# Kernel tuning notes

Measured on AMD Instinct MI355X. Metric: run time of the kernel, lower is better.

The kernel has to match this reference:

```python
import jax, jax.numpy as jnp
import numpy as np

NUM_EXPERTS = 8
CAPACITY_FACTOR = 1.0
MIN_CAPACITY = 4


def setup_inputs() -> dict:
    key = jax.random.key(0)
    k0, k1, k2, k3 = jax.random.split(key, 4)
    B, S, M, F, E = 4, 2048, 2048, 8192, NUM_EXPERTS
    return {
        "hidden_states": jax.random.normal(k0, (B, S, M), jnp.float32),
        "wg": jax.random.normal(k1, (M, E), jnp.float32) * 0.02,
        "w1": jax.random.normal(k2, (E, M, F), jnp.float32) * 0.02,
        "b1": jnp.zeros((E, F), jnp.float32),
        "w2": jax.random.normal(k3, (E, F, M), jnp.float32) * 0.02,
        "b2": jnp.zeros((E, M), jnp.float32),
    }


def reference(hidden_states, wg, w1, b1, w2, b2):
    B, S, M = hidden_states.shape
    E = NUM_EXPERTS
    T = B * S  # total tokens
    x = hidden_states.reshape(T, M)

    # ---- top-1 gating (DeepSpeed top1gating, no noise / no RTS) ----
    logits = x @ wg                                  # [T, E]
    gates = jax.nn.softmax(logits, axis=-1)          # [T, E]
    capacity = max(int(np.ceil(T / E * CAPACITY_FACTOR)), MIN_CAPACITY)

    idx1 = jnp.argmax(gates, axis=1)                 # [T]
    mask1 = jax.nn.one_hot(idx1, E, dtype=gates.dtype)  # [T, E]

    # position of each token within its expert's queue
    locations1 = jnp.cumsum(mask1, axis=0) - 1.0     # [T, E]

    # load-balancing aux loss (computed before capacity drop)
    me = jnp.mean(gates, axis=0)
    ce = jnp.mean(mask1, axis=0)
    l_aux = jnp.sum(me * ce) * E

    # drop tokens beyond capacity
    mask1 = mask1 * (locations1 < capacity).astype(mask1.dtype)
    locations1_s = jnp.sum(locations1 * mask1, axis=1).astype(jnp.int32)  # [T]

    gates1 = gates * mask1                           # [T, E], zero for dropped tokens
    loc_sc = jax.nn.one_hot(locations1_s, capacity, dtype=gates.dtype)    # [T, C]

    combine_weights = jnp.einsum("se,sc->sec", gates1, loc_sc)            # [T, E, C]
    dispatch_mask = (combine_weights > 0).astype(x.dtype)                  # [T, E, C]

    # ---- dispatch -> grouped-GEMM experts -> combine ----
    dispatched = jnp.einsum("sec,sm->ecm", dispatch_mask, x)              # [E, C, M]
    h = jax.nn.gelu(jnp.einsum("ecm,emf->ecf", dispatched, w1) + b1[:, None, :])
    expert_out = jnp.einsum("ecf,efm->ecm", h, w2) + b2[:, None, :]       # [E, C, M]

    out = jnp.einsum("sec,ecm->sm", combine_weights, expert_out)          # [T, M]
    return out.reshape(B, S, M), l_aux
```

## Files before the change

### kernel.cpp

```cpp
#include <hip/hip_runtime.h>
#include <hip/hip_bf16.h>
#include <math.h>

#define T_TOK 8192
#define M_DIM 2048
#define F_DIM 8192
#define E_NUM 8
#define CAP   1024

typedef unsigned short u16;
typedef __attribute__((ext_vector_type(8))) short short8;
typedef __attribute__((ext_vector_type(4))) float f32x4;

__device__ __forceinline__ u16 f2bf(float f){
  unsigned int x = __builtin_bit_cast(unsigned int, f);
  unsigned int lsb = (x >> 16) & 1u;
  x += 0x7fffu + lsb;
  return (u16)(x >> 16);
}
__device__ __forceinline__ unsigned int pack2(float a, float b){
  return (unsigned int)f2bf(a) | ((unsigned int)f2bf(b) << 16);
}

typedef __attribute__((address_space(3))) unsigned int lds_uint;
typedef __attribute__((address_space(1))) const unsigned int g_uint;
__device__ __forceinline__ void gl_lds16(const u16* g, u16* l){
  __builtin_amdgcn_global_load_lds((g_uint*)g, (lds_uint*)l, 16, 0, 0);
}
typedef __attribute__((address_space(3))) u16 lds_u16;
__device__ __forceinline__ unsigned int lds_off(u16* p){
  return (unsigned int)(unsigned long long)(lds_u16*)p;
}

__device__ __forceinline__ float gelu_tanh(float v){
  float u = 0.7978845608028654f * (v + 0.044715f * v * v * v);
  return 0.5f * v * (1.0f + tanhf(u));
}

__device__ __forceinline__ size_t tiled_off(int e, int n, int k, int nt128, int nkt){
  return ((((size_t)e * nt128 + (n >> 7)) * nkt + (k >> 6)) * 2 + ((k >> 5) & 1)) * 4096
         + (size_t)((n & 127) * 32 + ((((k >> 3) & 3) ^ ((n >> 1) & 3)) << 3) + (k & 7));
}

__global__ __launch_bounds__(256) void gating_kernel(
    const float* __restrict__ x, const float* __restrict__ wg,
    int* __restrict__ expert_id, float* __restrict__ gate_val,
    float* __restrict__ mepart)
{
  int wave = threadIdx.x >> 6, lane = threadIdx.x & 63;
  int t = blockIdx.x * 4 + wave;
  float acc[8];
  #pragma unroll
  for (int e = 0; e < 8; ++e) acc[e] = 0.f;
  const float* xr = x + (size_t)t * M_DIM;
  for (int i = lane; i < M_DIM; i += 64) {
    float xv = xr[i];
    const float4* wr = (const float4*)(wg + (size_t)i * 8);
    float4 w0 = wr[0], w1v = wr[1];
    acc[0] += xv * w0.x;  acc[1] += xv * w0.y;  acc[2] += xv * w0.z;  acc[3] += xv * w0.w;
    acc[4] += xv * w1v.x; acc[5] += xv * w1v.y; acc[6] += xv * w1v.z; acc[7] += xv * w1v.w;
  }
  #pragma unroll
  for (int off = 32; off; off >>= 1)
    #pragma unroll
    for (int e = 0; e < 8; ++e) acc[e] += __shfl_xor(acc[e], off);

  float mx = acc[0]; int bi = 0;
  #pragma unroll
  for (int e = 1; e < 8; ++e) if (acc[e] > mx) { mx = acc[e]; bi = e; }
  float p[8]; float s = 0.f;
  #pragma unroll
  for (int e = 0; e < 8; ++e) { p[e] = expf(acc[e] - mx); s += p[e]; }
  float inv = 1.f / s;

  __shared__ float pl[4][8];
  if (lane == 0) {
    expert_id[t] = bi;
    gate_val[t] = p[bi] * inv;
    #pragma unroll
    for (int e = 0; e < 8; ++e) pl[wave][e] = p[e] * inv;
  }
  __syncthreads();
  if (threadIdx.x < 8) {
    float m = pl[0][threadIdx.x] + pl[1][threadIdx.x] + pl[2][threadIdx.x] + pl[3][threadIdx.x];
    mepart[blockIdx.x * 8 + threadIdx.x] = m;
  }
}

__global__ __launch_bounds__(1024) void scan_kernel(
    const int* __restrict__ expert_id, const float* __restrict__ gate_val,
    const float* __restrict__ mepart, int nmep,
    int* __restrict__ slot_token, float* __restrict__ slot_gate,
    float* __restrict__ laux_out)
{
  __shared__ int wcnt[16][8];
  __shared__ int base[8];
  __shared__ float red[128][8];
  int tid = threadIdx.x, wave = tid >> 6, lane = tid & 63;
  if (tid < 8) base[tid] = 0;

  int e0 = tid & 7, g = tid >> 3;
  float mesum = 0.f;
  for (int r = g; r < nmep; r += 128) mesum += mepart[r * 8 + e0];
  red[g][e0] = mesum;
  __syncthreads();

  for (int tile = 0; tile < T_TOK / 1024; ++tile) {
    int t = tile * 1024 + tid;
    int e = expert_id[t];
    int lp = 0;
    #pragma unroll
    for (int ee = 0; ee < 8; ++ee) {
      unsigned long long m = __ballot(e == ee);
      if (lane == 0) wcnt[wave][ee] = __popcll(m);
      if (ee == e)   lp = __popcll(m & ((1ull << lane) - 1ull));
    }
    __syncthreads();
    int wp = 0;
    for (int w2 = 0; w2 < wave; ++w2) wp += wcnt[w2][e];
    int pos = base[e] + wp + lp;
    if (pos < CAP) {
      slot_token[e * CAP + pos] = t;
      slot_gate[e * CAP + pos] = gate_val[t];
    }
    __syncthreads();
    if (tid < 8) {
      int s = 0;
      for (int w2 = 0; w2 < 16; ++w2) s += wcnt[w2][tid];
      base[tid] += s;
    }
    __syncthreads();
  }

  if (tid < 8) {
    float me = 0.f;
    for (int r = 0; r < 128; ++r) me += red[r][tid];
    me /= (float)T_TOK;
    float ce = (float)base[tid] / (float)T_TOK;
    red[0][tid] = me * ce;
  }
  __syncthreads();
  if (tid == 0) {
    float s = 0.f;
    for (int e = 0; e < 8; ++e) s += red[0][e];
    *laux_out = s * (float)E_NUM;
  }
}

__global__ __launch_bounds__(256) void transpose_cvt_kernel(
    const float* __restrict__ in, u16* __restrict__ out, int R, int Cc)
{
  __shared__ float tile[64][65];
  int e = blockIdx.z;
  const float* ine = in + (size_t)e * R * Cc;
  int r0 = blockIdx.y * 64, c0 = blockIdx.x * 64;
  int tr = threadIdx.x >> 4, tc = threadIdx.x & 15;
  #pragma unroll
  for (int it = 0; it < 4; ++it) {
    float4 v = *(const float4*)&ine[(size_t)(r0 + it * 16 + tr) * Cc + c0 + tc * 4];
    tile[it * 16 + tr][tc * 4 + 0] = v.x;
    tile[it * 16 + tr][tc * 4 + 1] = v.y;
    tile[it * 16 + tr][tc * 4 + 2] = v.z;
    tile[it * 16 + tr][tc * 4 + 3] = v.w;
  }
  __syncthreads();
  int nt128 = Cc >> 7, nkt = R >> 6;
  int oc = threadIdx.x >> 2, q = threadIdx.x & 3;
  int n = c0 + oc, k0 = r0 + q * 16;
  u16 vals[16];
  #pragma unroll
  for (int i = 0; i < 16; ++i) vals[i] = f2bf(tile[q * 16 + i][oc]);
  unsigned int w[8];
  #pragma unroll
  for (int i = 0; i < 8; ++i) w[i] = (unsigned int)vals[2 * i] | ((unsigned int)vals[2 * i + 1] << 16);
  uint4 pa; pa.x = w[0]; pa.y = w[1]; pa.z = w[2]; pa.w = w[3];
  uint4 pb; pb.x = w[4]; pb.y = w[5]; pb.z = w[6]; pb.w = w[7];
  *(uint4*)&out[tiled_off(e, n, k0,     nt128, nkt)] = pa;
  *(uint4*)&out[tiled_off(e, n, k0 + 8, nt128, nkt)] = pb;
}

__global__ __launch_bounds__(256) void dispatch_kernel(
    const float* __restrict__ x, const int* __restrict__ slot_token,
    u16* __restrict__ Xe)
{
  int slot = blockIdx.x;
  int e = slot >> 10, c = slot & (CAP - 1);
  int t = slot_token[slot];
  int m = threadIdx.x * 8;
  uint4 pk;
  if (t < 0) {
    pk.x = pk.y = pk.z = pk.w = 0u;
  } else {
    const float* xr = x + (size_t)t * M_DIM + m;
    float4 a = *(const float4*)xr;
    float4 b = *(const float4*)(xr + 4);
    pk.x = pack2(a.x, a.y); pk.y = pack2(a.z, a.w);
    pk.z = pack2(b.x, b.y); pk.w = pack2(b.z, b.w);
  }
  *(uint4*)&Xe[tiled_off(e, c, m, CAP >> 7, M_DIM >> 6)] = pk;
}

template<int MH, int GATE>
__device__ __forceinline__ void do_phase(
    unsigned aAddr, unsigned bAddr,
    short8 (&bfr)[4], f32x4 (&acc)[4][4],
    const u16* __restrict__ tb, u16* sreg, int skt, int skh,
    int tid, int wave)
{
  short8 af[2];
  unsigned aA = aAddr + MH * 2048;
  if (MH == 0) {
    asm volatile("ds_read_b128 %0, %1 offset:0"    : "=v"(bfr[0]) : "v"(bAddr));
    asm volatile("ds_read_b128 %0, %1 offset:1024" : "=v"(bfr[1]) : "v"(bAddr));
    asm volatile("ds_read_b128 %0, %1 offset:2048" : "=v"(bfr[2]) : "v"(bAddr));
    asm volatile("ds_read_b128 %0, %1 offset:3072" : "=v"(bfr[3]) : "v"(bAddr));
  }
  asm volatile("ds_read_b128 %0, %1 offset:0"    : "=v"(af[0]) : "v"(aA));
  asm volatile("ds_read_b128 %0, %1 offset:1024" : "=v"(af[1]) : "v"(aA));
  const u16* src = tb + ((size_t)(skt * 2 + skh) << 12);
  #pragma unroll
  for (int j = 0; j < 2; ++j)
    gl_lds16(src + (size_t)(j * 256 + tid) * 8, sreg + (j * 256 + (wave << 6)) * 8);
  __builtin_amdgcn_s_barrier();
  asm volatile("s_waitcnt lgkmcnt(0)");
  __builtin_amdgcn_sched_barrier(0);
  __builtin_amdgcn_s_setprio(1);
  #pragma unroll
  for (int m2 = 0; m2 < 2; ++m2)
    #pragma unroll
    for (int n2 = 0; n2 < 4; ++n2)
      acc[MH * 2 + m2][n2] = __builtin_amdgcn_mfma_f32_16x16x32_bf16(
          af[m2], bfr[n2], acc[MH * 2 + m2][n2], 0, 0, 0);
  __builtin_amdgcn_s_setprio(0);
  if (GATE) {
    asm volatile("s_waitcnt vmcnt(6)");
    __builtin_amdgcn_sched_barrier(0);
  }
  __builtin_amdgcn_s_barrier();
}

template<int EPI>
__global__ __launch_bounds__(256, 2) void gemm8_kernel(
    const u16* __restrict__ A,
    const u16* __restrict__ B,
    const float* __restrict__ bias,
    u16* __restrict__ Hout,
    float* __restrict__ Out,
    const int* __restrict__ slot_token, const float* __restrict__ slot_gate,
    int K, int NR)
{
  __shared__ __align__(16) u16 SA[2][2][4096];
  __shared__ __align__(16) u16 SB[2][2][4096];

  int e = blockIdx.z;
  int n0 = blockIdx.x * 128, m0 = blockIdx.y * 128;
  int nkt = K >> 6;
  const u16* Atb = A + (((size_t)(e * (CAP >> 7) + (m0 >> 7)) * nkt) * 2) * 4096;
  const u16* Btb = B + (((size_t)(e * (NR >> 7) + (n0 >> 7)) * nkt) * 2) * 4096;

  int tid = threadIdx.x, wave = tid >> 6, lane = tid & 63;
  int wr = wave >> 1, wc = wave & 1;
  int l15 = lane & 15, g2 = lane >> 4;

  int rs = (l15 >> 1) & 3;
  int cg = (g2 ^ rs) * 8;
  int arow_base = (wr * 64 + l15) * 32 + cg;
  int brow_base = (wc * 64 + l15) * 32 + cg;

  unsigned aAddr[2][2], bAddr[2][2];
  #pragma unroll
  for (int b = 0; b < 2; ++b)
    #pragma unroll
    for (int h = 0; h < 2; ++h) {
      aAddr[b][h] = lds_off(&SA[b][h][0]) + (unsigned)(arow_base * 2);
      bAddr[b][h] = lds_off(&SB[b][h][0]) + (unsigned)(brow_base * 2);
    }

  f32x4 acc[4][4];
  #pragma unroll
  for (int m = 0; m < 4; ++m)
    #pragma unroll
    for (int n = 0; n < 4; ++n)
      acc[m][n] = (f32x4){0.f, 0.f, 0.f, 0.f};
  short8 bfr[4];

  auto stage0 = [&](const u16* tb, u16* region, int kt, int kh) {
    const u16* src = tb + ((size_t)(kt * 2 + kh) << 12);
    #pragma unroll
    for (int j = 0; j < 2; ++j)
      gl_lds16(src + (size_t)(j * 256 + tid) * 8, region + (j * 256 + (wave << 6)) * 8);
  };

  int nk = K >> 6, ni = nk >> 1;
  stage0(Btb, &SB[0][0][0], 0, 0);
  stage0(Atb, &SA[0][0][0], 0, 0);
  stage0(Btb, &SB[0][1][0], 0, 1);
  stage0(Atb, &SA[0][1][0], 0, 1);
  stage0(Btb, &SB[1][0][0], 1, 0);
  stage0(Atb, &SA[1][0][0], 1, 0);
  stage0(Btb, &SB[1][1][0], 1, 1);
  asm volatile("s_waitcnt vmcnt(6)");
  __builtin_amdgcn_sched_barrier(0);
  __builtin_amdgcn_s_barrier();

  #pragma unroll 1
  for (int i = 0; i < ni; ++i) {
    int t1 = 2 * i + 1;
    int t2 = 2 * i + 2 < nk ? 2 * i + 2 : nk - 1;
    int t3 = 2 * i + 3 < nk ? 2 * i + 3 : nk - 1;
    do_phase<0,0>(aAddr[0][0], bAddr[0][0], bfr, acc, Atb, &SA[1][1][0], t1, 1, tid, wave);
    do_phase<1,0>(aAddr[0][0], bAddr[0][0], bfr, acc, Btb, &SB[0][0][0], t2, 0, tid, wave);
    do_phase<0,0>(aAddr[0][1], bAddr[0][1], bfr, acc, Atb, &SA[0][0][0], t2, 0, tid, wave);
    do_phase<1,1>(aAddr[0][1], bAddr[0][1], bfr, acc, Btb, &SB[0][1][0], t2, 1, tid, wave);
    do_phase<0,0>(aAddr[1][0], bAddr[1][0], bfr, acc, Atb, &SA[0][1][0], t2, 1, tid, wave);
    do_phase<1,0>(aAddr[1][0], bAddr[1][0], bfr, acc, Btb, &SB[1][0][0], t3, 0, tid, wave);
    do_phase<0,0>(aAddr[1][1], bAddr[1][1], bfr, acc, Atb, &SA[1][0][0], t3, 0, tid, wave);
    do_phase<1,1>(aAddr[1][1], bAddr[1][1], bfr, acc, Btb, &SB[1][1][0], t3, 1, tid, wave);
  }

  int wrb = wr * 64, wcb = wc * 64;
  const float* be = bias + (size_t)e * NR + n0;
  if (EPI == 0) {
    #pragma unroll
    for (int wm = 0; wm < 4; ++wm) {
      #pragma unroll
      for (int j = 0; j < 4; ++j) {
        int r = wrb + wm * 16 + g2 * 4 + j;
        #pragma unroll
        for (int n = 0; n < 4; ++n) {
          int c = wcb + n * 16 + l15;
          float v = acc[wm][n][j] + be[c];
          Hout[tiled_off(e, m0 + r, n0 + c, CAP >> 7, F_DIM >> 6)] = f2bf(gelu_tanh(v));
        }
      }
    }
  } else {
    #pragma unroll
    for (int wm = 0; wm < 4; ++wm) {
      #pragma unroll
      for (int j = 0; j < 4; ++j) {
        int r = wrb + wm * 16 + g2 * 4 + j;
        int slot = e * CAP + m0 + r;
        int tk = slot_token[slot];
        if (tk >= 0) {
          float gv = slot_gate[slot];
          size_t rowoff = (size_t)tk * M_DIM + n0;
          #pragma unroll
          for (int n = 0; n < 4; ++n) {
            int c = wcb + n * 16 + l15;
            Out[rowoff + c] = gv * (acc[wm][n][j] + be[c]);
          }
        }
      }
    }
  }
}

extern "C" void kernel_launch(void* const* d_in, const int* in_sizes, int n_in,
                              void* d_out, int out_size, void* d_ws, size_t ws_size,
                              hipStream_t stream) {
  const float* x  = (const float*)d_in[0];
  const float* wg = (const float*)d_in[1];
  const float* w1 = (const float*)d_in[2];
  const float* b1 = (const float*)d_in[3];
  const float* w2 = (const float*)d_in[4];
  const float* b2 = (const float*)d_in[5];
  float* out = (float*)d_out;

  char* ws = (char*)d_ws;
  size_t o = 0;
  auto alloc = [&](size_t bytes) -> void* {
    void* p = ws + o;
    o += (bytes + 255) & ~(size_t)255;
    return p;
  };
  u16*   w1T        = (u16*)  alloc((size_t)E_NUM * F_DIM * M_DIM * 2);
  u16*   w2T        = (u16*)  alloc((size_t)E_NUM * M_DIM * F_DIM * 2);
  u16*   h          = (u16*)  alloc((size_t)E_NUM * CAP * F_DIM * 2);
  u16*   Xe         = (u16*)  alloc((size_t)E_NUM * CAP * M_DIM * 2);
  int*   expert_id  = (int*)  alloc(T_TOK * 4);
  float* gate_val   = (float*)alloc(T_TOK * 4);
  int*   slot_token = (int*)  alloc(E_NUM * CAP * 4);
  float* slot_gate  = (float*)alloc(E_NUM * CAP * 4);
  float* mepart     = (float*)alloc(2048 * 8 * 4);

  hipMemsetAsync(d_out, 0, (size_t)out_size * 4, stream);
  hipMemsetAsync(slot_token, 0xFF, E_NUM * CAP * 4, stream);

  gating_kernel<<<T_TOK / 4, 256, 0, stream>>>(x, wg, expert_id, gate_val, mepart);
  scan_kernel<<<1, 1024, 0, stream>>>(expert_id, gate_val, mepart, 2048,
                                      slot_token, slot_gate, out + (out_size - 1));
  transpose_cvt_kernel<<<dim3(128, 32, 8), 256, 0, stream>>>(w1, w1T, 2048, 8192);
  transpose_cvt_kernel<<<dim3(32, 128, 8), 256, 0, stream>>>(w2, w2T, 8192, 2048);
  dispatch_kernel<<<E_NUM * CAP, 256, 0, stream>>>(x, slot_token, Xe);

  gemm8_kernel<0><<<dim3(F_DIM / 128, CAP / 128, E_NUM), 256, 0, stream>>>(
      Xe, w1T, b1, h, nullptr, nullptr, nullptr, M_DIM, F_DIM);
  gemm8_kernel<1><<<dim3(M_DIM / 128, CAP / 128, E_NUM), 256, 0, stream>>>(
      h, w2T, b2, nullptr, out, slot_token, slot_gate, F_DIM, M_DIM);
}
```

Measured before the change: 1.018 ms.

## Halve GEMM LDS staging to double buffers and raise occupancy to four blocks

```diff
diff --git a/kernel.cpp b/kernel.cpp
--- a/kernel.cpp
+++ b/kernel.cpp
@@ -200,11 +200,11 @@
   *(uint4*)&Xe[tiled_off(e, c, m, CAP >> 7, M_DIM >> 6)] = pk;
 }
 
-template<int MH, int GATE>
+template<int MH>
 __device__ __forceinline__ void do_phase(
     unsigned aAddr, unsigned bAddr,
     short8 (&bfr)[4], f32x4 (&acc)[4][4],
-    const u16* __restrict__ tb, u16* sreg, int skt, int skh,
+    const u16* __restrict__ tb, u16* sreg, int skt,
     int tid, int wave)
 {
   short8 af[2];
@@ -217,7 +217,7 @@
   }
   asm volatile("ds_read_b128 %0, %1 offset:0"    : "=v"(af[0]) : "v"(aA));
   asm volatile("ds_read_b128 %0, %1 offset:1024" : "=v"(af[1]) : "v"(aA));
-  const u16* src = tb + ((size_t)(skt * 2 + skh) << 12);
+  const u16* src = tb + ((size_t)skt << 12);
   #pragma unroll
   for (int j = 0; j < 2; ++j)
     gl_lds16(src + (size_t)(j * 256 + tid) * 8, sreg + (j * 256 + (wave << 6)) * 8);
@@ -232,15 +232,15 @@
       acc[MH * 2 + m2][n2] = __builtin_amdgcn_mfma_f32_16x16x32_bf16(
           af[m2], bfr[n2], acc[MH * 2 + m2][n2], 0, 0, 0);
   __builtin_amdgcn_s_setprio(0);
-  if (GATE) {
-    asm volatile("s_waitcnt vmcnt(6)");
+  if (MH == 1) {
+    asm volatile("s_waitcnt vmcnt(2)");
     __builtin_amdgcn_sched_barrier(0);
   }
   __builtin_amdgcn_s_barrier();
 }
 
 template<int EPI>
-__global__ __launch_bounds__(256, 2) void gemm8_kernel(
+__global__ __launch_bounds__(256, 4) void gemm8_kernel(
     const u16* __restrict__ A,
     const u16* __restrict__ B,
     const float* __restrict__ bias,
@@ -249,14 +249,14 @@
     const int* __restrict__ slot_token, const float* __restrict__ slot_gate,
     int K, int NR)
 {
-  __shared__ __align__(16) u16 SA[2][2][4096];
-  __shared__ __align__(16) u16 SB[2][2][4096];
+  __shared__ __align__(16) u16 SA[2][4096];
+  __shared__ __align__(16) u16 SB[2][4096];
 
   int e = blockIdx.z;
   int n0 = blockIdx.x * 128, m0 = blockIdx.y * 128;
-  int nkt = K >> 6;
-  const u16* Atb = A + (((size_t)(e * (CAP >> 7) + (m0 >> 7)) * nkt) * 2) * 4096;
-  const u16* Btb = B + (((size_t)(e * (NR >> 7) + (n0 >> 7)) * nkt) * 2) * 4096;
+  int nreg = K >> 5;
+  const u16* Atb = A + ((size_t)(e * (CAP >> 7) + (m0 >> 7)) * nreg) * 4096;
+  const u16* Btb = B + ((size_t)(e * (NR >> 7) + (n0 >> 7)) * nreg) * 4096;
 
   int tid = threadIdx.x, wave = tid >> 6, lane = tid & 63;
   int wr = wave >> 1, wc = wave & 1;
@@ -267,14 +267,12 @@
   int arow_base = (wr * 64 + l15) * 32 + cg;
   int brow_base = (wc * 64 + l15) * 32 + cg;
 
-  unsigned aAddr[2][2], bAddr[2][2];
-  #pragma unroll
-  for (int b = 0; b < 2; ++b)
-    #pragma unroll
-    for (int h = 0; h < 2; ++h) {
-      aAddr[b][h] = lds_off(&SA[b][h][0]) + (unsigned)(arow_base * 2);
-      bAddr[b][h] = lds_off(&SB[b][h][0]) + (unsigned)(brow_base * 2);
-    }
+  unsigned aAddr[2], bAddr[2];
+  #pragma unroll
+  for (int b = 0; b < 2; ++b) {
+    aAddr[b] = lds_off(&SA[b][0]) + (unsigned)(arow_base * 2);
+    bAddr[b] = lds_off(&SB[b][0]) + (unsigned)(brow_base * 2);
+  }
 
   f32x4 acc[4][4];
   #pragma unroll
@@ -284,38 +282,28 @@
       acc[m][n] = (f32x4){0.f, 0.f, 0.f, 0.f};
   short8 bfr[4];
 
-  auto stage0 = [&](const u16* tb, u16* region, int kt, int kh) {
-    const u16* src = tb + ((size_t)(kt * 2 + kh) << 12);
+  auto stageR = [&](const u16* tb, u16* region, int kt) {
+    const u16* src = tb + ((size_t)kt << 12);
     #pragma unroll
     for (int j = 0; j < 2; ++j)
       gl_lds16(src + (size_t)(j * 256 + tid) * 8, region + (j * 256 + (wave << 6)) * 8);
   };
 
-  int nk = K >> 6, ni = nk >> 1;
-  stage0(Btb, &SB[0][0][0], 0, 0);
-  stage0(Atb, &SA[0][0][0], 0, 0);
-  stage0(Btb, &SB[0][1][0], 0, 1);
-  stage0(Atb, &SA[0][1][0], 0, 1);
-  stage0(Btb, &SB[1][0][0], 1, 0);
-  stage0(Atb, &SA[1][0][0], 1, 0);
-  stage0(Btb, &SB[1][1][0], 1, 1);
-  asm volatile("s_waitcnt vmcnt(6)");
+  int nk = K >> 5;
+  stageR(Atb, &SA[0][0], 0);
+  stageR(Btb, &SB[0][0], 0);
+  stageR(Btb, &SB[1][0], 1);
+  asm volatile("s_waitcnt vmcnt(2)");
   __builtin_amdgcn_sched_barrier(0);
   __builtin_amdgcn_s_barrier();
 
   #pragma unroll 1
-  for (int i = 0; i < ni; ++i) {
-    int t1 = 2 * i + 1;
-    int t2 = 2 * i + 2 < nk ? 2 * i + 2 : nk - 1;
-    int t3 = 2 * i + 3 < nk ? 2 * i + 3 : nk - 1;
-    do_phase<0,0>(aAddr[0][0], bAddr[0][0], bfr, acc, Atb, &SA[1][1][0], t1, 1, tid, wave);
-    do_phase<1,0>(aAddr[0][0], bAddr[0][0], bfr, acc, Btb, &SB[0][0][0], t2, 0, tid, wave);
-    do_phase<0,0>(aAddr[0][1], bAddr[0][1], bfr, acc, Atb, &SA[0][0][0], t2, 0, tid, wave);
-    do_phase<1,1>(aAddr[0][1], bAddr[0][1], bfr, acc, Btb, &SB[0][1][0], t2, 1, tid, wave);
-    do_phase<0,0>(aAddr[1][0], bAddr[1][0], bfr, acc, Atb, &SA[0][1][0], t2, 1, tid, wave);
-    do_phase<1,0>(aAddr[1][0], bAddr[1][0], bfr, acc, Btb, &SB[1][0][0], t3, 0, tid, wave);
-    do_phase<0,0>(aAddr[1][1], bAddr[1][1], bfr, acc, Atb, &SA[1][0][0], t3, 0, tid, wave);
-    do_phase<1,1>(aAddr[1][1], bAddr[1][1], bfr, acc, Btb, &SB[1][1][0], t3, 1, tid, wave);
+  for (int t = 0; t < nk; ++t) {
+    int p = t & 1;
+    int tA = t + 1 < nk ? t + 1 : nk - 1;
+    int tB = t + 2 < nk ? t + 2 : nk - 1;
+    do_phase<0>(aAddr[p], bAddr[p], bfr, acc, Atb, &SA[p ^ 1][0], tA, tid, wave);
+    do_phase<1>(aAddr[p], bAddr[p], bfr, acc, Btb, &SB[p][0], tB, tid, wave);
   }
 
   int wrb = wr * 64, wcb = wc * 64;
```

Result: faster. 981.2 us (-3.6%).
